# Performance work log

Hardware: AMD Instinct MI355X
Metric: run time of the kernel (lower is better)

Reference implementation:

```python
import jax, jax.numpy as jnp
import numpy as np

B, T, V, C, NB = 8, 2048, 1024, 128, 32


def setup_inputs() -> dict:
    key = jax.random.key(0)
    ks = jax.random.split(key, 6)
    x = jax.random.normal(ks[0], (B, T, V), jnp.float32)
    basis = jax.random.normal(ks[1], (V, 2 * NB), jnp.float32)
    q_coeffs = jax.random.normal(ks[2], (C, 2 * NB), jnp.float32) * 0.02
    k_coeffs = jax.random.normal(ks[3], (C, 2 * NB), jnp.float32) * 0.02
    v_coeffs = jax.random.normal(ks[4], (C, 2 * NB), jnp.float32) * 0.02
    o_coeffs = jax.random.normal(ks[5], (C, 2 * NB), jnp.float32) * 0.02
    decay = jnp.float32(0.95)
    out_scale = jnp.float32(0.1)
    return {"x": x, "basis": basis, "q_coeffs": q_coeffs, "k_coeffs": k_coeffs,
            "v_coeffs": v_coeffs, "o_coeffs": o_coeffs, "decay": decay, "out_scale": out_scale}


def reference(x, basis, q_coeffs, k_coeffs, v_coeffs, o_coeffs, decay, out_scale):
    # Fourier-parameterized projections: (V, C); softmax over vocab dim for q/k/v
    q_w = jax.nn.softmax(basis @ q_coeffs.T, axis=0)
    k_w = jax.nn.softmax(basis @ k_coeffs.T, axis=0)
    v_w = jax.nn.softmax(basis @ v_coeffs.T, axis=0)
    o_w = basis @ o_coeffs.T  # (V, C), no softmax

    q = x @ q_w  # (B, T, C)
    k = x @ k_w
    v = x @ v_w
    d = jax.nn.sigmoid(decay)

    M0 = jnp.zeros((x.shape[0], q_w.shape[1], q_w.shape[1]), x.dtype)  # (B, C, C)

    def step(M, qkv_t):
        q_t, k_t, v_t = qkv_t  # each (B, C)
        retrieved = jnp.einsum('bc,bcd->bd', q_t, M)  # read BEFORE write (as in torch loop)
        M_new = d * M + jnp.einsum('bc,bd->bcd', k_t, v_t)
        return M_new, retrieved

    qT = jnp.swapaxes(q, 0, 1)  # (T, B, C)
    kT = jnp.swapaxes(k, 0, 1)
    vT = jnp.swapaxes(v, 0, 1)
    _, rs = jax.lax.scan(step, M0, (qT, kT, vT))  # rs: (T, B, C)
    retrieved = jnp.swapaxes(rs, 0, 1)  # (B, T, C)
    return (retrieved @ o_w.T) * out_scale  # (B, T, V)
```

## Files before the change

kernel.cpp:

```cpp
#include <hip/hip_runtime.h>
#include <math.h>

#define B_   8
#define T_   2048
#define V_   1024
#define C_   128
#define NB2  64
#define L_   32
#define NC_  64

typedef _Float16 f16_t;
typedef f16_t f16x8 __attribute__((ext_vector_type(8)));
typedef float f32x4 __attribute__((ext_vector_type(4)));

__device__ __forceinline__ float sigmoidf_(float x){ return 1.0f/(1.0f+expf(-x)); }

__device__ __forceinline__ void gload_lds16(const void* g, void* l){
  __builtin_amdgcn_global_load_lds(
      (const __attribute__((address_space(1))) uint32_t*)g,
      (__attribute__((address_space(3))) uint32_t*)l, 16, 0, 0);
}

__global__ __launch_bounds__(256) void weights_kernel(
    const float* __restrict__ basis,
    const float* __restrict__ qc, const float* __restrict__ kc,
    const float* __restrict__ vc, const float* __restrict__ oc,
    f16_t* __restrict__ Wo, f16_t* __restrict__ Wt)
{
  int blk  = blockIdx.x;
  int proj = blk >> 7;
  int c    = blk & 127;
  const float* coeffs = (proj==0)?qc : (proj==1)?kc : (proj==2)?vc : oc;

  __shared__ float coef[NB2];
  __shared__ float red[256];
  int tid = threadIdx.x;
  if (tid < NB2) coef[tid] = coeffs[c*NB2 + tid];
  __syncthreads();

  float l[4];
  for (int i=0;i<4;i++){
    int v = tid + i*256;
    const float4* bp = (const float4*)(basis + (size_t)v*NB2);
    float s = 0.f;
    #pragma unroll
    for (int f=0; f<NB2/4; f++){
      float4 b4 = bp[f];
      s += b4.x*coef[f*4+0] + b4.y*coef[f*4+1] + b4.z*coef[f*4+2] + b4.w*coef[f*4+3];
    }
    l[i] = s;
  }
  if (proj == 3){
    for (int i=0;i<4;i++){ int v = tid+i*256; Wo[(size_t)v*C_ + c] = (f16_t)l[i]; }
    return;
  }
  float mx = fmaxf(fmaxf(l[0],l[1]), fmaxf(l[2],l[3]));
  red[tid] = mx; __syncthreads();
  for (int s=128; s>0; s>>=1){ if (tid<s) red[tid] = fmaxf(red[tid], red[tid+s]); __syncthreads(); }
  mx = red[0]; __syncthreads();
  float sum = 0.f;
  for (int i=0;i<4;i++) sum += expf(l[i]-mx);
  red[tid] = sum; __syncthreads();
  for (int s=128; s>0; s>>=1){ if (tid<s) red[tid] += red[tid+s]; __syncthreads(); }
  float inv = 1.0f/red[0];
  f16_t* tp = Wt + ((size_t)proj*C_ + c)*V_;
  for (int i=0;i<4;i++){
    int v = tid+i*256;
    tp[v] = (f16_t)(expf(l[i]-mx)*inv);
  }
}

#define BM 64
#define BN 128
#define BK 64
#define PADK 72
#define NF_  384
#define NT_PROJ (V_/BK)

__global__ __launch_bounds__(512, 1) void proj_fused_kernel(
    const float* __restrict__ x,
    const f16_t* __restrict__ Wt,
    float* __restrict__ out)
{
  const int M = B_*T_;
  int m0 = blockIdx.x * BM;

  __shared__ __align__(16) f16_t As[BM][PADK];
  __shared__ __align__(16) f16_t Bsh[NF_*BK];

  int tid  = threadIdx.x;
  int lane = tid & 63;
  int w    = tid >> 6;
  int wm   = (w >> 2) * 32;
  int wn   = (w & 3) * 96;
  int lr   = lane & 15;
  int lg   = lane >> 4;

  const float* xbase = x + (size_t)m0*V_;

  f32x4 acc[2][6] = {};

  for (int kt = 0; kt < NT_PROJ; kt++){
    #pragma unroll
    for (int i=0;i<6;i++){
      int ci = i*512 + tid;
      int r  = ci >> 3, ch = ci & 7;
      const f16_t* src = Wt + (size_t)r*V_ + kt*BK + ((ch ^ (r&7))<<3);
      gload_lds16(src, &Bsh[ci*8]);
    }
    #pragma unroll
    for (int i=0;i<2;i++){
      int ci = i*512 + tid;
      int row = ci >> 4, q = ci & 15;
      float4 xv = *(const float4*)(xbase + (size_t)row*V_ + kt*BK + q*4);
      union { f16_t h[4]; ushort4 u; } hh;
      hh.h[0]=(f16_t)xv.x; hh.h[1]=(f16_t)xv.y; hh.h[2]=(f16_t)xv.z; hh.h[3]=(f16_t)xv.w;
      *(ushort4*)&As[row][q*4] = hh.u;
    }
    __syncthreads();

    #pragma unroll
    for (int kh=0; kh<2; kh++){
      f16x8 a[2];
      #pragma unroll
      for (int mt=0; mt<2; mt++)
        a[mt] = *(f16x8*)&As[wm + mt*16 + lr][kh*32 + lg*8];
      #pragma unroll
      for (int nt=0; nt<6; nt++){
        int n  = wn + nt*16 + lr;
        int c0 = kh*4 + lg;
        f16x8 b = *(f16x8*)&Bsh[n*BK + ((c0 ^ (n&7))<<3)];
        #pragma unroll
        for (int mt=0; mt<2; mt++)
          acc[mt][nt] = __builtin_amdgcn_mfma_f32_16x16x32_f16(a[mt], b, acc[mt][nt], 0,0,0);
      }
    }
    __syncthreads();
  }

  #pragma unroll
  for (int mt=0; mt<2; mt++)
    #pragma unroll
    for (int nt=0; nt<6; nt++){
      int n   = wn + nt*16 + lr;
      int p   = n >> 7;
      int col = n & 127;
      float* op = out + (size_t)p*M*C_;
      #pragma unroll
      for (int r=0; r<4; r++){
        int row = m0 + wm + mt*16 + lg*4 + r;
        op[(size_t)row*C_ + col] = acc[mt][nt][r];
      }
    }
}

__global__ __launch_bounds__(256) void kvsum_kernel(
    const float* __restrict__ k, const float* __restrict__ v,
    const float* __restrict__ dptr, float* __restrict__ kv)
{
  int ci = blockIdx.x, b = blockIdx.y;
  float d = sigmoidf_(dptr[0]);
  __shared__ float ks[L_][132];
  __shared__ float vs[L_][132];
  int tid = threadIdx.x;
  const float* kp = k + ((size_t)b*T_ + ci*L_)*C_;
  const float* vp = v + ((size_t)b*T_ + ci*L_)*C_;
  #pragma unroll
  for (int i=0;i<4;i++){
    int idx = tid + i*256;
    int j = idx >> 5, c4 = idx & 31;
    float w = powf(d, (float)(L_-1-j));
    float4 k4 = *(const float4*)(kp + (size_t)j*C_ + c4*4);
    k4.x*=w; k4.y*=w; k4.z*=w; k4.w*=w;
    *(float4*)&ks[j][c4*4] = k4;
    *(float4*)&vs[j][c4*4] = *(const float4*)(vp + (size_t)j*C_ + c4*4);
  }
  __syncthreads();
  int tc = tid >> 4, td = tid & 15;
  float acc[8][8] = {};
  for (int j=0;j<L_;j++){
    float kr[8], vr[8];
    *(float4*)&kr[0] = *(float4*)&ks[j][tc*8];
    *(float4*)&kr[4] = *(float4*)&ks[j][tc*8+4];
    *(float4*)&vr[0] = *(float4*)&vs[j][td*8];
    *(float4*)&vr[4] = *(float4*)&vs[j][td*8+4];
    #pragma unroll
    for (int a=0;a<8;a++)
      #pragma unroll
      for (int bb=0;bb<8;bb++) acc[a][bb] += kr[a]*vr[bb];
  }
  float* op = kv + ((size_t)b*NC_ + ci)*C_*C_;
  for (int a=0;a<8;a++)
    for (int b4=0;b4<2;b4++)
      *(float4*)(op + (size_t)(tc*8+a)*C_ + td*8 + b4*4) =
        make_float4(acc[a][b4*4],acc[a][b4*4+1],acc[a][b4*4+2],acc[a][b4*4+3]);
}

__global__ __launch_bounds__(256) void scan_kernel(
    float* __restrict__ kv, const float* __restrict__ dptr)
{
  int idx = blockIdx.x*256 + threadIdx.x;
  int b = idx >> 14, e = idx & 16383;
  float d  = sigmoidf_(dptr[0]);
  float dL = powf(d, (float)L_);
  float* p = kv + (size_t)b*NC_*C_*C_ + e;
  float m = 0.f;
  for (int i=0;i<NC_;i++){
    float s = p[(size_t)i*C_*C_];
    p[(size_t)i*C_*C_] = m;
    m = dL*m + s;
  }
}

__global__ __launch_bounds__(256) void intra_kernel(
    const float* __restrict__ q, const float* __restrict__ k,
    const float* __restrict__ v, const float* __restrict__ Minit,
    const float* __restrict__ dptr,
    f16_t* __restrict__ ret)
{
  int ci = blockIdx.x, b = blockIdx.y;
  int tid = threadIdx.x;
  float d = sigmoidf_(dptr[0]);
  __shared__ float qs[L_][132];
  __shared__ float kvs[L_][132];
  __shared__ __align__(16) float Ms[C_][C_];
  __shared__ float ps[L_][33];
  __shared__ float dpow[L_+1];
  if (tid <= L_) dpow[tid] = powf(d, (float)tid);

  const float* qp = q + ((size_t)b*T_ + ci*L_)*C_;
  const float* kp = k + ((size_t)b*T_ + ci*L_)*C_;
  const float* vp = v + ((size_t)b*T_ + ci*L_)*C_;
  const float* Mp = Minit + ((size_t)b*NC_ + ci)*C_*C_;

  #pragma unroll
  for (int i=0;i<16;i++){
    int cidx = i*256 + tid;
    gload_lds16(Mp + (size_t)cidx*4, &Ms[0][0] + cidx*4);
  }
  #pragma unroll
  for (int i=0;i<4;i++){
    int idx = tid + i*256;
    int j = idx >> 5, c4 = idx & 31;
    *(float4*)&qs[j][c4*4]  = *(const float4*)(qp + (size_t)j*C_ + c4*4);
    *(float4*)&kvs[j][c4*4] = *(const float4*)(kp + (size_t)j*C_ + c4*4);
  }
  __syncthreads();

  {
    int tr = tid >> 4, tj = tid & 15;
    float s[2][2] = {};
    for (int c4=0;c4<32;c4++){
      float4 q4[2], k4[2];
      #pragma unroll
      for (int i=0;i<2;i++) q4[i] = *(float4*)&qs[tr*2+i][c4*4];
      #pragma unroll
      for (int i=0;i<2;i++) k4[i] = *(float4*)&kvs[tj*2+i][c4*4];
      #pragma unroll
      for (int a=0;a<2;a++)
        #pragma unroll
        for (int bb=0;bb<2;bb++)
          s[a][bb] += q4[a].x*k4[bb].x + q4[a].y*k4[bb].y + q4[a].z*k4[bb].z + q4[a].w*k4[bb].w;
    }
    #pragma unroll
    for (int a=0;a<2;a++)
      #pragma unroll
      for (int bb=0;bb<2;bb++){
        int r = tr*2+a, j = tj*2+bb;
        ps[r][j] = (j < r) ? s[a][bb]*dpow[r-1-j] : 0.f;
      }
  }
  __syncthreads();

  #pragma unroll
  for (int i=0;i<4;i++){
    int idx = tid + i*256;
    int j = idx >> 5, c4 = idx & 31;
    *(float4*)&kvs[j][c4*4] = *(const float4*)(vp + (size_t)j*C_ + c4*4);
  }

  int tx = tid & 31, ty = tid >> 5;
  float acc[4][4] = {};
  for (int c=0;c<C_;c++){
    float4 m4 = *(const float4*)&Ms[c][tx*4];
    #pragma unroll
    for (int r=0;r<4;r++){
      float qv = qs[ty*4+r][c];
      acc[r][0] += qv*m4.x; acc[r][1] += qv*m4.y; acc[r][2] += qv*m4.z; acc[r][3] += qv*m4.w;
    }
  }
  #pragma unroll
  for (int r=0;r<4;r++){
    float sc = dpow[ty*4+r];
    #pragma unroll
    for (int j=0;j<4;j++) acc[r][j] *= sc;
  }
  __syncthreads();

  for (int j=0;j<L_;j++){
    float4 v4 = *(float4*)&kvs[j][tx*4];
    #pragma unroll
    for (int r=0;r<4;r++){
      float p = ps[ty*4+r][j];
      acc[r][0] += p*v4.x; acc[r][1] += p*v4.y; acc[r][2] += p*v4.z; acc[r][3] += p*v4.w;
    }
  }
  size_t rbase = ((size_t)b*T_ + ci*L_)*C_;
  for (int r=0;r<4;r++){
    union { f16_t h[4]; ushort4 u; } hh;
    #pragma unroll
    for (int j=0;j<4;j++) hh.h[j] = (f16_t)acc[r][j];
    *(ushort4*)(ret + rbase + (size_t)(ty*4+r)*C_ + tx*4) = hh.u;
  }
}

__global__ __launch_bounds__(256) void out_mfma_kernel(
    const f16_t* __restrict__ A, const f16_t* __restrict__ Bw,
    const float* __restrict__ scl, float* __restrict__ out)
{
  int m0 = blockIdx.x * BM;
  int n0 = blockIdx.y * BN;
  float osc = scl[0];

  int tid  = threadIdx.x;
  int lane = tid & 63;
  int w    = tid >> 6;
  int wm   = (w >> 1) * 32;
  int wn   = (w & 1) * 64;
  int lr   = lane & 15;
  int lg   = lane >> 4;

  f32x4 acc[2][4] = {};

  #pragma unroll
  for (int kh=0; kh<4; kh++){
    f16x8 a[2];
    #pragma unroll
    for (int mt=0; mt<2; mt++)
      a[mt] = *(const f16x8*)(A + (size_t)(m0 + wm + mt*16 + lr)*C_ + kh*32 + lg*8);
    #pragma unroll
    for (int nt=0; nt<4; nt++){
      f16x8 bfr = *(const f16x8*)(Bw + (size_t)(n0 + wn + nt*16 + lr)*C_ + kh*32 + lg*8);
      #pragma unroll
      for (int mt=0; mt<2; mt++)
        acc[mt][nt] = __builtin_amdgcn_mfma_f32_16x16x32_f16(a[mt], bfr, acc[mt][nt], 0,0,0);
    }
  }

  #pragma unroll
  for (int mt=0; mt<2; mt++)
    #pragma unroll
    for (int nt=0; nt<4; nt++)
      #pragma unroll
      for (int r=0; r<4; r++){
        int row = m0 + wm + mt*16 + lg*4 + r;
        int col = n0 + wn + nt*16 + lr;
        out[(size_t)row*V_ + col] = acc[mt][nt][r] * osc;
      }
}

extern "C" void kernel_launch(void* const* d_in, const int* in_sizes, int n_in,
                              void* d_out, int out_size, void* d_ws, size_t ws_size,
                              hipStream_t stream)
{
  const float* x     = (const float*)d_in[0];
  const float* basis = (const float*)d_in[1];
  const float* qc    = (const float*)d_in[2];
  const float* kc    = (const float*)d_in[3];
  const float* vc    = (const float*)d_in[4];
  const float* oc    = (const float*)d_in[5];
  const float* dptr  = (const float*)d_in[6];
  const float* sptr  = (const float*)d_in[7];
  float* out = (float*)d_out;
  float* ws  = (float*)d_ws;

  const size_t M = (size_t)B_*T_;
  f16_t* Wo  = (f16_t*)ws;
  f16_t* Wt  = (f16_t*)(ws + 65536);
  float* qkv = ws + 262144;
  f16_t* ret = (f16_t*)(ws + 6553600);
  float* kv  = ws + 7602176;

  float* q = qkv;
  float* k = qkv + M*C_;
  float* v = qkv + 2*M*C_;

  hipLaunchKernelGGL(weights_kernel, dim3(512), dim3(256), 0, stream,
                     basis, qc, kc, vc, oc, Wo, Wt);
  hipLaunchKernelGGL(proj_fused_kernel, dim3(256), dim3(512), 0, stream,
                     x, Wt, qkv);
  hipLaunchKernelGGL(kvsum_kernel, dim3(NC_, B_), dim3(256), 0, stream, k, v, dptr, kv);
  hipLaunchKernelGGL(scan_kernel, dim3(512), dim3(256), 0, stream, kv, dptr);
  hipLaunchKernelGGL(intra_kernel, dim3(NC_, B_), dim3(256), 0, stream,
                     q, k, v, kv, dptr, ret);
  hipLaunchKernelGGL(out_mfma_kernel, dim3(256, 8), dim3(256), 0, stream,
                     ret, Wo, sptr, out);
}
```

Before: 258.8 us.

## Fuse per-chunk KV outer-product sums into projection GEMM epilogue

The projection GEMM epilogue now also writes the scaled k and unscaled v tiles into shared memory, reusing the GEMM staging buffers, and computes the per-chunk k^T v sums for its two 32-row chunks. This removes the separate kvsum kernel launch and its re-read of k and v from global memory. The scan loop is also manually unrolled by four to batch its loads. In exchange, the fused kernel gets a longer serial tail with an extra barrier, and it only runs 256 blocks, so parallelism in the kv phase is lower than in the old standalone kernel.

```diff
diff --git a/kernel.cpp b/kernel.cpp
--- a/kernel.cpp
+++ b/kernel.cpp
@@ -76,17 +76,24 @@
 #define PADK 72
 #define NF_  384
 #define NT_PROJ (V_/BK)
+#define KVPAD 132
 
 __global__ __launch_bounds__(512, 1) void proj_fused_kernel(
     const float* __restrict__ x,
     const f16_t* __restrict__ Wt,
-    float* __restrict__ out)
+    const float* __restrict__ dptr,
+    float* __restrict__ out,
+    float* __restrict__ kv)
 {
   const int M = B_*T_;
   int m0 = blockIdx.x * BM;
 
-  __shared__ __align__(16) f16_t As[BM][PADK];
-  __shared__ __align__(16) f16_t Bsh[NF_*BK];
+  __shared__ __align__(16) float pool[16896];
+  __shared__ float dpow[L_];
+  f16_t* As  = (f16_t*)pool;
+  f16_t* Bsh = (f16_t*)pool + 64*PADK;
+  float* ks  = pool;
+  float* vs  = pool + 8448;
 
   int tid  = threadIdx.x;
   int lane = tid & 63;
@@ -96,6 +103,9 @@
   int lr   = lane & 15;
   int lg   = lane >> 4;
 
+  float d = sigmoidf_(dptr[0]);
+  if (tid < L_) dpow[tid] = powf(d, (float)tid);
+
   const float* xbase = x + (size_t)m0*V_;
 
   f32x4 acc[2][6] = {};
@@ -111,11 +121,11 @@
     #pragma unroll
     for (int i=0;i<2;i++){
       int ci = i*512 + tid;
-      int row = ci >> 4, q = ci & 15;
-      float4 xv = *(const float4*)(xbase + (size_t)row*V_ + kt*BK + q*4);
+      int row = ci >> 4, qq = ci & 15;
+      float4 xv = *(const float4*)(xbase + (size_t)row*V_ + kt*BK + qq*4);
       union { f16_t h[4]; ushort4 u; } hh;
       hh.h[0]=(f16_t)xv.x; hh.h[1]=(f16_t)xv.y; hh.h[2]=(f16_t)xv.z; hh.h[3]=(f16_t)xv.w;
-      *(ushort4*)&As[row][q*4] = hh.u;
+      *(ushort4*)&As[row*PADK + qq*4] = hh.u;
     }
     __syncthreads();
 
@@ -124,7 +134,7 @@
       f16x8 a[2];
       #pragma unroll
       for (int mt=0; mt<2; mt++)
-        a[mt] = *(f16x8*)&As[wm + mt*16 + lr][kh*32 + lg*8];
+        a[mt] = *(f16x8*)&As[(wm + mt*16 + lr)*PADK + kh*32 + lg*8];
       #pragma unroll
       for (int nt=0; nt<6; nt++){
         int n  = wn + nt*16 + lr;
@@ -148,52 +158,44 @@
       float* op = out + (size_t)p*M*C_;
       #pragma unroll
       for (int r=0; r<4; r++){
-        int row = m0 + wm + mt*16 + lg*4 + r;
-        op[(size_t)row*C_ + col] = acc[mt][nt][r];
+        int row64 = wm + mt*16 + lg*4 + r;
+        float val = acc[mt][nt][r];
+        op[(size_t)(m0 + row64)*C_ + col] = val;
+        int chnk = row64 >> 5, jrow = row64 & 31;
+        if (p == 1)
+          ks[chnk*(L_*KVPAD) + jrow*KVPAD + col] = val * dpow[L_-1-jrow];
+        else if (p == 2)
+          vs[chnk*(L_*KVPAD) + jrow*KVPAD + col] = val;
       }
     }
-}
-
-__global__ __launch_bounds__(256) void kvsum_kernel(
-    const float* __restrict__ k, const float* __restrict__ v,
-    const float* __restrict__ dptr, float* __restrict__ kv)
-{
-  int ci = blockIdx.x, b = blockIdx.y;
-  float d = sigmoidf_(dptr[0]);
-  __shared__ float ks[L_][132];
-  __shared__ float vs[L_][132];
-  int tid = threadIdx.x;
-  const float* kp = k + ((size_t)b*T_ + ci*L_)*C_;
-  const float* vp = v + ((size_t)b*T_ + ci*L_)*C_;
-  #pragma unroll
-  for (int i=0;i<4;i++){
-    int idx = tid + i*256;
-    int j = idx >> 5, c4 = idx & 31;
-    float w = powf(d, (float)(L_-1-j));
-    float4 k4 = *(const float4*)(kp + (size_t)j*C_ + c4*4);
-    k4.x*=w; k4.y*=w; k4.z*=w; k4.w*=w;
-    *(float4*)&ks[j][c4*4] = k4;
-    *(float4*)&vs[j][c4*4] = *(const float4*)(vp + (size_t)j*C_ + c4*4);
-  }
   __syncthreads();
-  int tc = tid >> 4, td = tid & 15;
-  float acc[8][8] = {};
-  for (int j=0;j<L_;j++){
-    float kr[8], vr[8];
-    *(float4*)&kr[0] = *(float4*)&ks[j][tc*8];
-    *(float4*)&kr[4] = *(float4*)&ks[j][tc*8+4];
-    *(float4*)&vr[0] = *(float4*)&vs[j][td*8];
-    *(float4*)&vr[4] = *(float4*)&vs[j][td*8+4];
-    #pragma unroll
+
+  {
+    int chnk = tid >> 8;
+    int t2   = tid & 255;
+    int tc   = t2 >> 4, td = t2 & 15;
+    const float* ksp = ks + chnk*(L_*KVPAD);
+    const float* vsp = vs + chnk*(L_*KVPAD);
+    float a8[8][8] = {};
+    for (int j=0;j<L_;j++){
+      float kr[8], vr[8];
+      *(float4*)&kr[0] = *(const float4*)&ksp[j*KVPAD + tc*8];
+      *(float4*)&kr[4] = *(const float4*)&ksp[j*KVPAD + tc*8+4];
+      *(float4*)&vr[0] = *(const float4*)&vsp[j*KVPAD + td*8];
+      *(float4*)&vr[4] = *(const float4*)&vsp[j*KVPAD + td*8+4];
+      #pragma unroll
+      for (int a=0;a<8;a++)
+        #pragma unroll
+        for (int bb=0;bb<8;bb++) a8[a][bb] += kr[a]*vr[bb];
+    }
+    int bb_  = m0 >> 11;
+    int ci0  = (m0 & (T_-1)) >> 5;
+    float* op2 = kv + ((size_t)bb_*NC_ + ci0 + chnk)*C_*C_;
     for (int a=0;a<8;a++)
-      #pragma unroll
-      for (int bb=0;bb<8;bb++) acc[a][bb] += kr[a]*vr[bb];
-  }
-  float* op = kv + ((size_t)b*NC_ + ci)*C_*C_;
-  for (int a=0;a<8;a++)
-    for (int b4=0;b4<2;b4++)
-      *(float4*)(op + (size_t)(tc*8+a)*C_ + td*8 + b4*4) =
-        make_float4(acc[a][b4*4],acc[a][b4*4+1],acc[a][b4*4+2],acc[a][b4*4+3]);
+      for (int b4=0;b4<2;b4++)
+        *(float4*)(op2 + (size_t)(tc*8+a)*C_ + td*8 + b4*4) =
+          make_float4(a8[a][b4*4],a8[a][b4*4+1],a8[a][b4*4+2],a8[a][b4*4+3]);
+  }
 }
 
 __global__ __launch_bounds__(256) void scan_kernel(
@@ -204,11 +206,18 @@
   float d  = sigmoidf_(dptr[0]);
   float dL = powf(d, (float)L_);
   float* p = kv + (size_t)b*NC_*C_*C_ + e;
+  const size_t S = (size_t)C_*C_;
   float m = 0.f;
-  for (int i=0;i<NC_;i++){
-    float s = p[(size_t)i*C_*C_];
-    p[(size_t)i*C_*C_] = m;
-    m = dL*m + s;
+  #pragma unroll 4
+  for (int g=0; g<NC_/4; g++){
+    float s0 = p[(size_t)(4*g+0)*S];
+    float s1 = p[(size_t)(4*g+1)*S];
+    float s2 = p[(size_t)(4*g+2)*S];
+    float s3 = p[(size_t)(4*g+3)*S];
+    p[(size_t)(4*g+0)*S] = m;  m = dL*m + s0;
+    p[(size_t)(4*g+1)*S] = m;  m = dL*m + s1;
+    p[(size_t)(4*g+2)*S] = m;  m = dL*m + s2;
+    p[(size_t)(4*g+3)*S] = m;  m = dL*m + s3;
   }
 }
 
@@ -388,8 +397,7 @@
   hipLaunchKernelGGL(weights_kernel, dim3(512), dim3(256), 0, stream,
                      basis, qc, kc, vc, oc, Wo, Wt);
   hipLaunchKernelGGL(proj_fused_kernel, dim3(256), dim3(512), 0, stream,
-                     x, Wt, qkv);
-  hipLaunchKernelGGL(kvsum_kernel, dim3(NC_, B_), dim3(256), 0, stream, k, v, dptr, kv);
+                     x, Wt, dptr, qkv, kv);
   hipLaunchKernelGGL(scan_kernel, dim3(512), dim3(256), 0, stream, kv, dptr);
   hipLaunchKernelGGL(intra_kernel, dim3(NC_, B_), dim3(256), 0, stream,
                      q, k, v, kv, dptr, ret);
```

Result: no change. 255.1 us (-1.4%).
